# Kernel tuning notes

Hardware: AMD Instinct MI355X
Metric: run time of the kernel (lower is better)

The kernel has to match this reference:

```python
import jax, jax.numpy as jnp
import numpy as np
from jax import lax

B, C_IN, C_OUT, K, W, H = 2, 64, 64, 9, 192, 192
EXTEND_SCOPE = 1.0
EPS = 1e-5
GN_GROUPS = C_OUT // 4


def setup_inputs() -> dict:
    key = jax.random.key(0)
    ks = jax.random.split(key, 6)
    f = jax.random.normal(ks[0], (B, C_IN, W, H), jnp.float32)
    offset_w = jax.random.normal(ks[1], (2 * K, C_IN, 3, 3), jnp.float32) * 0.02
    offset_b = jax.random.normal(ks[2], (2 * K,), jnp.float32) * 0.02
    bn_gamma = jnp.ones((2 * K,), jnp.float32)
    bn_beta = jnp.zeros((2 * K,), jnp.float32)
    conv_w = jax.random.normal(ks[3], (C_OUT, C_IN, K, 1), jnp.float32) * 0.05
    conv_b = jax.random.normal(ks[4], (C_OUT,), jnp.float32) * 0.05
    gn_gamma = jnp.ones((C_OUT,), jnp.float32)
    gn_beta = jnp.zeros((C_OUT,), jnp.float32)
    return dict(f=f, offset_w=offset_w, offset_b=offset_b, bn_gamma=bn_gamma,
                bn_beta=bn_beta, conv_w=conv_w, conv_b=conv_b,
                gn_gamma=gn_gamma, gn_beta=gn_beta)


def _forward(f, offset_w, offset_b, bn_gamma, bn_beta, conv_w, conv_b, gn_gamma, gn_beta):
    # --- offset branch: 3x3 conv -> eval-mode BatchNorm -> tanh ---
    off = lax.conv_general_dilated(f, offset_w, (1, 1), [(1, 1), (1, 1)],
                                   dimension_numbers=('NCHW', 'OIHW', 'NCHW'))
    off = off + offset_b[None, :, None, None]
    # BN eval: running_mean=0, running_var=1
    off = off / jnp.sqrt(1.0 + EPS) * bn_gamma[None, :, None, None] + bn_beta[None, :, None, None]
    off = jnp.tanh(off)
    y_off = off[:, :K]  # [B,K,W,H]; x_off (off[:, K:]) is unused when morph == 0

    # --- cumulative snake offsets along the kernel axis (morph=0 uses y only) ---
    center = K // 2
    # faithful to source: tensor starts as a detached clone; entries never
    # reassigned by the loop (index 0 and K-1 for odd K) keep raw detached offsets
    new = [lax.stop_gradient(y_off[:, i]) for i in range(K)]
    new[center] = jnp.zeros_like(new[center])
    for j in range(1, center):
        new[center + j] = new[center + j - 1] + y_off[:, center + j]
        new[center - j] = new[center - j + 1] + y_off[:, center - j]
    y_off_cum = jnp.stack(new, axis=1)  # [B,K,W,H]

    # --- deformed sampling coordinates ---
    w_idx = jnp.arange(W, dtype=jnp.float32)[None, None, :, None]
    h_idx = jnp.arange(H, dtype=jnp.float32)[None, None, None, :]
    k_off = (jnp.arange(K, dtype=jnp.float32) - center)[None, :, None, None]
    y_new = w_idx + EXTEND_SCOPE * y_off_cum              # [B,K,W,H]
    x_new = jnp.broadcast_to(h_idx + k_off, (B, K, W, H))  # [B,K,W,H]
    # torch layout: [B,K,W,H] -> [B,W,K,H] -> [B, K*W, H]
    yf = y_new.transpose(0, 2, 1, 3).reshape(-1)
    xf = x_new.transpose(0, 2, 1, 3).reshape(-1)

    # --- bilinear interpolation gather ---
    y0 = jnp.floor(yf)
    x0 = jnp.floor(xf)
    y0i = jnp.clip(y0.astype(jnp.int32), 0, W - 1)
    y1i = jnp.clip(y0.astype(jnp.int32) + 1, 0, W - 1)
    x0i = jnp.clip(x0.astype(jnp.int32), 0, H - 1)
    x1i = jnp.clip(x0.astype(jnp.int32) + 1, 0, H - 1)

    # faithful to source: base batch offset cancels, so every batch gathers
    # from batch 0's feature map
    feat0 = f[0].transpose(1, 2, 0).reshape(W * H, C_IN)  # [(w,h), C]
    va0 = feat0[y0i * H + x0i]
    vc0 = feat0[y0i * H + x1i]
    va1 = feat0[y1i * H + x0i]
    vc1 = feat0[y1i * H + x1i]

    # interpolation weights use the looser clamp [0, W] / [0, H] (source behavior)
    y0w = jnp.clip(y0, 0.0, float(W))
    y1w = jnp.clip(y0 + 1.0, 0.0, float(W))
    x0w = jnp.clip(x0, 0.0, float(H))
    x1w = jnp.clip(x0 + 1.0, 0.0, float(H))
    wa0 = (y1w - yf) * (x1w - xf)
    wc0 = (y1w - yf) * (xf - x0w)
    wa1 = (yf - y0w) * (x1w - xf)
    wc1 = (yf - y0w) * (xf - x0w)
    vals = va0 * wa0[:, None] + vc0 * wc0[:, None] + va1 * wa1[:, None] + vc1 * wc1[:, None]
    deformed = vals.reshape(B, K * W, H, C_IN).transpose(0, 3, 1, 2)  # [B,C,K*W,H]

    # --- dsc_conv_x: (K,1) kernel, (K,1) stride -> [B,C_out,W,H] ---
    z = lax.conv_general_dilated(deformed, conv_w, (K, 1), 'VALID',
                                 dimension_numbers=('NCHW', 'OIHW', 'NCHW'))
    z = z + conv_b[None, :, None, None]

    # --- GroupNorm(out_ch//4, out_ch) + ReLU ---
    zg = z.reshape(B, GN_GROUPS, -1)
    mu = zg.mean(axis=-1, keepdims=True)
    var = zg.var(axis=-1, keepdims=True)
    zg = (zg - mu) / jnp.sqrt(var + EPS)
    z = zg.reshape(B, C_OUT, W, H) * gn_gamma[None, :, None, None] + gn_beta[None, :, None, None]
    return jax.nn.relu(z)


def reference(f, offset_w, offset_b, bn_gamma, bn_beta, conv_w, conv_b, gn_gamma, gn_beta):
    return _forward(f, offset_w, offset_b, bn_gamma, bn_beta, conv_w, conv_b, gn_gamma, gn_beta)
```

## Files before the change

kernel.cpp:

```cpp
#include <hip/hip_runtime.h>

#define BB 2
#define CIN 64
#define COUT 64
#define KK 9
#define WW 192
#define HH 192
#define WH (WW*HH)
#define CENTER 4
#define NT 32
#define DEFP 584
#define GROUPS 16
constexpr float EPSV = 1e-5f;
constexpr int NPERG = 4 * WH;

typedef __attribute__((ext_vector_type(8))) short short8v;
typedef __attribute__((ext_vector_type(4))) float float4v;

__device__ __forceinline__ float bf2f(unsigned short u) {
    union { unsigned int i; float f; } x; x.i = ((unsigned int)u) << 16; return x.f;
}
__device__ __forceinline__ unsigned short f2bf(float f) {
    union { float f; unsigned int i; } x; x.f = f;
    unsigned int i = x.i;
    unsigned int r = i + 0x7FFFu + ((i >> 16) & 1u);
    return (unsigned short)(r >> 16);
}

__global__ void k_prep(const float* __restrict__ cw, const float* __restrict__ ow,
                       unsigned short* __restrict__ wtA, float* __restrict__ wl_g)
{
    int i = blockIdx.x * 256 + threadIdx.x;
    if (i < COUT * CIN * KK) {
        int o = i / 576, ck = i % 576;
        int k = ck >> 6, c = ck & 63;
        wtA[i] = f2bf(cw[o * 576 + c * 9 + k]);
    }
    int j2 = i - COUT * CIN * KK;
    if (j2 >= 0 && j2 < CIN * 9 * 12) {
        int c = j2 / 108, rem = j2 % 108, tap = rem / 12, jj = rem % 12;
        wl_g[j2] = (jj < 9) ? ow[jj * 576 + c * 9 + tap] : 0.f;
    }
}

__global__ __launch_bounds__(256) void k_tr(const float* __restrict__ f,
                                            unsigned short* __restrict__ f_t)
{
    __shared__ unsigned short tile[64][72];
    int tid = threadIdx.x;
    int y = blockIdx.y;
    int x0 = blockIdx.x * 64;
    int xl = tid & 63, cq = tid >> 6;
#pragma unroll
    for (int ci = 0; ci < 16; ++ci) {
        int c = cq * 16 + ci;
        tile[xl][c] = f2bf(f[c * WH + y * HH + x0 + xl]);
    }
    __syncthreads();
    int cp = tid & 31, xr0 = tid >> 5;
#pragma unroll
    for (int xi = 0; xi < 8; ++xi) {
        int xr = xr0 * 8 + xi;
        unsigned int val = (unsigned int)tile[xr][2 * cp] |
                           ((unsigned int)tile[xr][2 * cp + 1] << 16);
        ((unsigned int*)f_t)[(y * HH + x0 + xr) * 32 + cp] = val;
    }
}

__global__ __launch_bounds__(256) void k_fused(
    const float* __restrict__ f, const unsigned short* __restrict__ f_t,
    const float* __restrict__ wl_g, const unsigned short* __restrict__ wtA,
    const float* __restrict__ ob, const float* __restrict__ bg,
    const float* __restrict__ bb, const float* __restrict__ cb,
    float* __restrict__ zout)
{
    __shared__ float4 wl4[1728];
    __shared__ unsigned short def[NT * DEFP];
    __shared__ short m_y0[KK * NT], m_y1[KK * NT], m_x[KK * NT];
    __shared__ float m_w0[KK * NT], m_w1[KK * NT];
    float* wl = (float*)wl4;
    float* part = (float*)def;

    int tid = threadIdx.x;
    int h0 = blockIdx.x * NT;
    int w = blockIdx.y;
    int b = blockIdx.z;
    int lane = tid & 63;
    int wid = tid >> 6;
    int lr = lane & 15;
    int lg = lane >> 4;
    int o0 = wid * 16;

    for (int i = tid; i < 1728; i += 256)
        wl4[i] = ((const float4*)wl_g)[i];

    int p = tid & 31, c8 = tid >> 5;
    float acc[9];
#pragma unroll
    for (int j = 0; j < 9; ++j) acc[j] = 0.f;
    const float* fb = f + ((size_t)b * CIN + c8 * 8) * WH;
    __syncthreads();

#pragma unroll
    for (int tap = 0; tap < 9; ++tap) {
        int r = w + tap / 3 - 1;
        int cl = h0 + p + tap % 3 - 1;
        if ((unsigned)r >= WW || (unsigned)cl >= HH) continue;
        const float* src = fb + r * HH + cl;
#pragma unroll
        for (int cc = 0; cc < 8; ++cc) {
            float v = src[cc * WH];
            const float* ww = wl + (c8 * 8 + cc) * 108 + tap * 12;
            float4 wa = *(const float4*)ww;
            float4 wb2 = *(const float4*)(ww + 4);
            float w8 = ww[8];
            acc[0] += v * wa.x;  acc[1] += v * wa.y;
            acc[2] += v * wa.z;  acc[3] += v * wa.w;
            acc[4] += v * wb2.x; acc[5] += v * wb2.y;
            acc[6] += v * wb2.z; acc[7] += v * wb2.w;
            acc[8] += v * w8;
        }
    }
#pragma unroll
    for (int j = 0; j < 9; ++j)
        part[(c8 * 32 + p) * 9 + j] = acc[j];

    short8v afr[18];
    const unsigned short* wbase = wtA + (o0 + lr) * 576 + lg * 8;
#pragma unroll
    for (int s = 0; s < 18; ++s)
        afr[s] = *(const short8v*)(wbase + s * 32);
    __syncthreads();

    if (tid < NT) {
        float s[9];
#pragma unroll
        for (int j = 0; j < 9; ++j) {
            float t0 = 0.f;
#pragma unroll
            for (int g = 0; g < 8; ++g) t0 += part[(g * 32 + tid) * 9 + j];
            s[j] = t0;
        }
        const float inv = 1.0f / sqrtf(1.0f + EPSV);
        float t[9];
#pragma unroll
        for (int j = 0; j < 9; ++j)
            t[j] = tanhf((s[j] + ob[j]) * inv * bg[j] + bb[j]);
        float cum[9];
        cum[4] = 0.f;
        cum[5] = t[5]; cum[6] = cum[5] + t[6]; cum[7] = cum[6] + t[7];
        cum[3] = t[3]; cum[2] = cum[3] + t[2]; cum[1] = cum[2] + t[1];
        cum[0] = t[0]; cum[8] = t[8];
        int h = h0 + tid;
#pragma unroll
        for (int k = 0; k < 9; ++k) {
            float yf = cum[k] + (float)w;
            int x = h + k - CENTER;
            float y0f = floorf(yf);
            int iy0 = (int)y0f;
            int y0i = min(max(iy0, 0), WW - 1);
            int y1i = min(max(iy0 + 1, 0), WW - 1);
            float y0w = fminf(fmaxf(y0f, 0.f), (float)WW);
            float y1w = fminf(fmaxf(y0f + 1.f, 0.f), (float)WW);
            float w0 = y1w - yf;
            float w1 = yf - y0w;
            if (x < 0 || x >= HH) { w0 = 0.f; w1 = 0.f; }
            int pp = k * NT + tid;
            m_y0[pp] = (short)y0i;
            m_y1[pp] = (short)y1i;
            m_x[pp]  = (short)min(max(x, 0), HH - 1);
            m_w0[pp] = w0;
            m_w1[pp] = w1;
        }
    }
    __syncthreads();

    for (int it = tid; it < KK * NT * 4; it += 256) {
        int q = it & 3;
        int pp = it >> 2;
        int y0i = m_y0[pp], y1i = m_y1[pp], x = m_x[pp];
        float w0 = m_w0[pp], w1 = m_w1[pp];
        const unsigned short* r0 = f_t + ((y0i * HH + x) << 6) + q * 16;
        const unsigned short* r1 = f_t + ((y1i * HH + x) << 6) + q * 16;
        short8v a0 = *(const short8v*)r0;
        short8v a1 = *(const short8v*)(r0 + 8);
        short8v c0 = *(const short8v*)r1;
        short8v c1 = *(const short8v*)(r1 + 8);
        short8v o0v, o1v;
#pragma unroll
        for (int c = 0; c < 8; ++c) {
            float v0 = bf2f((unsigned short)a0[c]) * w0 + bf2f((unsigned short)c0[c]) * w1;
            float v1 = bf2f((unsigned short)a1[c]) * w0 + bf2f((unsigned short)c1[c]) * w1;
            o0v[c] = (short)f2bf(v0);
            o1v[c] = (short)f2bf(v1);
        }
        int hl = pp & 31;
        int k = pp >> 5;
        unsigned short* d = &def[hl * DEFP + k * 64 + q * 16];
        *(short8v*)d = o0v;
        *(short8v*)(d + 8) = o1v;
    }
    __syncthreads();

    float4v acc0 = {0.f, 0.f, 0.f, 0.f};
    float4v acc1 = {0.f, 0.f, 0.f, 0.f};
    const unsigned short* drow0 = &def[lr * DEFP + lg * 8];
    const unsigned short* drow1 = &def[(16 + lr) * DEFP + lg * 8];
#pragma unroll
    for (int s = 0; s < 18; ++s) {
        short8v b0 = *(const short8v*)(drow0 + s * 32);
        short8v b1 = *(const short8v*)(drow1 + s * 32);
        acc0 = __builtin_amdgcn_mfma_f32_16x16x32_bf16(afr[s], b0, acc0, 0, 0, 0);
        acc1 = __builtin_amdgcn_mfma_f32_16x16x32_bf16(afr[s], b1, acc1, 0, 0, 0);
    }

    float4 cbv = *(const float4*)(cb + o0 + lg * 4);
    size_t base = ((size_t)(b * COUT + o0 + lg * 4) * WW + w) * HH + h0 + lr;
#pragma unroll
    for (int r = 0; r < 4; ++r) {
        float bias = (r == 0) ? cbv.x : (r == 1) ? cbv.y : (r == 2) ? cbv.z : cbv.w;
        zout[base + (size_t)r * WH]      = acc0[r] + bias;
        zout[base + (size_t)r * WH + 16] = acc1[r] + bias;
    }
}

__global__ __launch_bounds__(1024) void k_gstats(const float* __restrict__ z,
                                                 float* __restrict__ ms)
{
    __shared__ float sL[16], qL[16];
    int b = blockIdx.x >> 4, g = blockIdx.x & 15;
    const float4* p = (const float4*)(z + ((size_t)b * COUT + g * 4) * WH);
    float s = 0.f, q = 0.f;
    for (int i = threadIdx.x; i < WH; i += 1024) {
        float4 v = p[i];
        s += v.x + v.y + v.z + v.w;
        q += v.x * v.x + v.y * v.y + v.z * v.z + v.w * v.w;
    }
#pragma unroll
    for (int m = 1; m < 64; m <<= 1) {
        s += __shfl_xor(s, m);
        q += __shfl_xor(q, m);
    }
    int wv = threadIdx.x >> 6;
    if ((threadIdx.x & 63) == 0) { sL[wv] = s; qL[wv] = q; }
    __syncthreads();
    if (threadIdx.x == 0) {
        float ts = 0.f, tq = 0.f;
#pragma unroll
        for (int i = 0; i < 16; ++i) { ts += sL[i]; tq += qL[i]; }
        float mean = ts / (float)NPERG;
        float var = tq / (float)NPERG - mean * mean;
        ms[b * GROUPS + g] = mean;
        ms[BB * GROUPS + b * GROUPS + g] = 1.0f / sqrtf(var + EPSV);
    }
}

__global__ __launch_bounds__(256) void k_norm(
    float* __restrict__ z, const float* __restrict__ ms,
    const float* __restrict__ gg, const float* __restrict__ gb)
{
    int i = blockIdx.x * 256 + threadIdx.x;
    const int total4 = BB * COUT * WH / 4;
    if (i >= total4) return;
    float4 v = ((float4*)z)[i];
    int idx = i * 4;
    int o = (idx / WH) % COUT;
    int b = idx / (COUT * WH);
    int g = o >> 2;
    float mean = ms[b * GROUPS + g];
    float istd = ms[BB * GROUPS + b * GROUPS + g];
    float ga = gg[o], be = gb[o];
    v.x = fmaxf((v.x - mean) * istd * ga + be, 0.f);
    v.y = fmaxf((v.y - mean) * istd * ga + be, 0.f);
    v.z = fmaxf((v.z - mean) * istd * ga + be, 0.f);
    v.w = fmaxf((v.w - mean) * istd * ga + be, 0.f);
    ((float4*)z)[i] = v;
}

extern "C" void kernel_launch(void* const* d_in, const int* in_sizes, int n_in,
                              void* d_out, int out_size, void* d_ws, size_t ws_size,
                              hipStream_t stream)
{
    const float* f  = (const float*)d_in[0];
    const float* ow = (const float*)d_in[1];
    const float* ob = (const float*)d_in[2];
    const float* bg = (const float*)d_in[3];
    const float* bb = (const float*)d_in[4];
    const float* cw = (const float*)d_in[5];
    const float* cb = (const float*)d_in[6];
    const float* gg = (const float*)d_in[7];
    const float* gb = (const float*)d_in[8];
    float* out = (float*)d_out;

    char* ws = (char*)d_ws;
    unsigned short* f_t = (unsigned short*)ws;
    unsigned short* wtA = (unsigned short*)(ws + 4718592);
    float* wl_g         = (float*)(ws + 4718592 + 73728);
    float* ms           = (float*)(ws + 4718592 + 73728 + 27648);

    k_prep<<<(36864 + 6912 + 255) / 256, 256, 0, stream>>>(cw, ow, wtA, wl_g);
    k_tr<<<dim3(3, WW), 256, 0, stream>>>(f, f_t);
    k_fused<<<dim3(HH / NT, WW, BB), 256, 0, stream>>>(f, f_t, wl_g, wtA, ob, bg, bb, cb, out);
    k_gstats<<<BB * GROUPS, 1024, 0, stream>>>(out, ms);
    k_norm<<<(BB * COUT * WH / 4 + 255) / 256, 256, 0, stream>>>(out, ms, gg, gb);
}
```

Before: 187.9 us.

## Fuse GroupNorm partial statistics into conv epilogue and remap block order

The fused conv kernel now reduces per-block sums and sums of squares for each GroupNorm group and writes them to a small partial-stats buffer. The stats kernel then reduces those partials instead of re-reading the full output tensor, removing one full pass over z. The grid also becomes 1D with a swizzled block-to-(w,h,b) mapping that interleaves blocks across XCD chunks, aiming at better cache locality. The partial sums are in fp32 and reduced in a different order, which slightly changes numerics.

```diff
diff --git a/kernel.cpp b/kernel.cpp
--- a/kernel.cpp
+++ b/kernel.cpp
@@ -11,6 +11,7 @@
 #define NT 32
 #define DEFP 584
 #define GROUPS 16
+#define NBLK 2304
 constexpr float EPSV = 1e-5f;
 constexpr int NPERG = 4 * WH;
 
@@ -72,7 +73,7 @@
     const float* __restrict__ wl_g, const unsigned short* __restrict__ wtA,
     const float* __restrict__ ob, const float* __restrict__ bg,
     const float* __restrict__ bb, const float* __restrict__ cb,
-    float* __restrict__ zout)
+    float* __restrict__ zout, float* __restrict__ pstats)
 {
     __shared__ float4 wl4[1728];
     __shared__ unsigned short def[NT * DEFP];
@@ -82,9 +83,13 @@
     float* part = (float*)def;
 
     int tid = threadIdx.x;
-    int h0 = blockIdx.x * NT;
-    int w = blockIdx.y;
-    int b = blockIdx.z;
+    int pb = blockIdx.x;
+    int xc = pb & 7;
+    int j = pb >> 3;
+    int w = xc * 24 + (j % 24);
+    int h0 = ((j / 24) % 6) * NT;
+    int b = j / 144;
+
     int lane = tid & 63;
     int wid = tid >> 6;
     int lr = lane & 15;
@@ -97,7 +102,7 @@
     int p = tid & 31, c8 = tid >> 5;
     float acc[9];
 #pragma unroll
-    for (int j = 0; j < 9; ++j) acc[j] = 0.f;
+    for (int jj = 0; jj < 9; ++jj) acc[jj] = 0.f;
     const float* fb = f + ((size_t)b * CIN + c8 * 8) * WH;
     __syncthreads();
 
@@ -122,8 +127,8 @@
         }
     }
 #pragma unroll
-    for (int j = 0; j < 9; ++j)
-        part[(c8 * 32 + p) * 9 + j] = acc[j];
+    for (int jj = 0; jj < 9; ++jj)
+        part[(c8 * 32 + p) * 9 + jj] = acc[jj];
 
     short8v afr[18];
     const unsigned short* wbase = wtA + (o0 + lr) * 576 + lg * 8;
@@ -135,17 +140,17 @@
     if (tid < NT) {
         float s[9];
 #pragma unroll
-        for (int j = 0; j < 9; ++j) {
+        for (int jj = 0; jj < 9; ++jj) {
             float t0 = 0.f;
 #pragma unroll
-            for (int g = 0; g < 8; ++g) t0 += part[(g * 32 + tid) * 9 + j];
-            s[j] = t0;
+            for (int g = 0; g < 8; ++g) t0 += part[(g * 32 + tid) * 9 + jj];
+            s[jj] = t0;
         }
         const float inv = 1.0f / sqrtf(1.0f + EPSV);
         float t[9];
 #pragma unroll
-        for (int j = 0; j < 9; ++j)
-            t[j] = tanhf((s[j] + ob[j]) * inv * bg[j] + bb[j]);
+        for (int jj = 0; jj < 9; ++jj)
+            t[jj] = tanhf((s[jj] + ob[jj]) * inv * bg[jj] + bb[jj]);
         float cum[9];
         cum[4] = 0.f;
         cum[5] = t[5]; cum[6] = cum[5] + t[6]; cum[7] = cum[6] + t[7];
@@ -215,26 +220,42 @@
     }
 
     float4 cbv = *(const float4*)(cb + o0 + lg * 4);
+    float lsum = 0.f, lsq = 0.f;
     size_t base = ((size_t)(b * COUT + o0 + lg * 4) * WW + w) * HH + h0 + lr;
 #pragma unroll
     for (int r = 0; r < 4; ++r) {
         float bias = (r == 0) ? cbv.x : (r == 1) ? cbv.y : (r == 2) ? cbv.z : cbv.w;
-        zout[base + (size_t)r * WH]      = acc0[r] + bias;
-        zout[base + (size_t)r * WH + 16] = acc1[r] + bias;
-    }
-}
-
-__global__ __launch_bounds__(1024) void k_gstats(const float* __restrict__ z,
+        float z0 = acc0[r] + bias;
+        float z1 = acc1[r] + bias;
+        zout[base + (size_t)r * WH]      = z0;
+        zout[base + (size_t)r * WH + 16] = z1;
+        lsum += z0 + z1;
+        lsq  += z0 * z0 + z1 * z1;
+    }
+#pragma unroll
+    for (int m = 1; m < 16; m <<= 1) {
+        lsum += __shfl_xor(lsum, m);
+        lsq  += __shfl_xor(lsq, m);
+    }
+    if (lr == 0) {
+        int g = wid * 4 + lg;
+        pstats[(size_t)pb * 32 + g]      = lsum;
+        pstats[(size_t)pb * 32 + 16 + g] = lsq;
+    }
+}
+
+__global__ __launch_bounds__(1024) void k_stats2(const float* __restrict__ pstats,
                                                  float* __restrict__ ms)
 {
     __shared__ float sL[16], qL[16];
     int b = blockIdx.x >> 4, g = blockIdx.x & 15;
-    const float4* p = (const float4*)(z + ((size_t)b * COUT + g * 4) * WH);
     float s = 0.f, q = 0.f;
-    for (int i = threadIdx.x; i < WH; i += 1024) {
-        float4 v = p[i];
-        s += v.x + v.y + v.z + v.w;
-        q += v.x * v.x + v.y * v.y + v.z * v.z + v.w * v.w;
+    for (int pb = threadIdx.x; pb < NBLK; pb += 1024) {
+        int bb = (pb >> 3) / 144;
+        if (bb == b) {
+            s += pstats[(size_t)pb * 32 + g];
+            q += pstats[(size_t)pb * 32 + 16 + g];
+        }
     }
 #pragma unroll
     for (int m = 1; m < 64; m <<= 1) {
@@ -296,11 +317,12 @@
     unsigned short* f_t = (unsigned short*)ws;
     unsigned short* wtA = (unsigned short*)(ws + 4718592);
     float* wl_g         = (float*)(ws + 4718592 + 73728);
-    float* ms           = (float*)(ws + 4718592 + 73728 + 27648);
+    float* pstats       = (float*)(ws + 4718592 + 73728 + 27648);
+    float* ms           = (float*)(ws + 4718592 + 73728 + 27648 + 294912);
 
     k_prep<<<(36864 + 6912 + 255) / 256, 256, 0, stream>>>(cw, ow, wtA, wl_g);
     k_tr<<<dim3(3, WW), 256, 0, stream>>>(f, f_t);
-    k_fused<<<dim3(HH / NT, WW, BB), 256, 0, stream>>>(f, f_t, wl_g, wtA, ob, bg, bb, cb, out);
-    k_gstats<<<BB * GROUPS, 1024, 0, stream>>>(out, ms);
+    k_fused<<<NBLK, 256, 0, stream>>>(f, f_t, wl_g, wtA, ob, bg, bb, cb, out, pstats);
+    k_stats2<<<BB * GROUPS, 1024, 0, stream>>>(pstats, ms);
     k_norm<<<(BB * COUT * WH / 4 + 255) / 256, 256, 0, stream>>>(out, ms, gg, gb);
 }
```

Result: faster. 165.3 us (-12.0%).
